# Optimization experiments

Hardware: AMD Instinct MI355X
Metric: run time of the kernel (lower is better)

The kernel has to match this reference:

```python
import jax, jax.numpy as jnp
import numpy as np

FEAT_STRIDE = 16
PRE_NMS_TOP_N = 4000
POST_NMS_TOP_N = 300
NMS_THRESH = 0.7


def _whctrs(a):
    w = a[2] - a[0] + 1.0
    h = a[3] - a[1] + 1.0
    return w, h, a[0] + 0.5 * (w - 1.0), a[1] + 0.5 * (h - 1.0)

def _mkanchors(ws, hs, xc, yc):
    ws = ws[:, None]; hs = hs[:, None]
    return np.hstack([xc - 0.5 * (ws - 1), yc - 0.5 * (hs - 1), xc + 0.5 * (ws - 1), yc + 0.5 * (hs - 1)])

def _ratio_enum(anchor, ratios):
    w, h, xc, yc = _whctrs(anchor)
    size = w * h
    ws = np.round(np.sqrt(size / ratios))
    hs = np.round(ws * ratios)
    return _mkanchors(ws, hs, xc, yc)

def _scale_enum(anchor, scales):
    w, h, xc, yc = _whctrs(anchor)
    return _mkanchors(w * scales, h * scales, xc, yc)

def generate_anchors(base_size, ratios, scales):
    base = np.array([1.0, 1.0, base_size, base_size], dtype=np.float64) - 1.0
    ra = _ratio_enum(base, np.asarray(ratios, dtype=np.float64))
    return np.vstack([_scale_enum(ra[i], np.asarray(scales, dtype=np.float64)) for i in range(ra.shape[0])]).astype(np.float32)

# ---- NMS: sequential greedy suppression over score-sorted boxes ----

def _nms_keep(boxes, thresh):
    # boxes: [N,4] sorted by descending score. Legacy +1 area convention.
    boxes = jax.lax.stop_gradient(boxes)
    x1, y1, x2, y2 = boxes[:, 0], boxes[:, 1], boxes[:, 2], boxes[:, 3]
    areas = (x2 - x1 + 1.0) * (y2 - y1 + 1.0)
    xx1 = jnp.maximum(x1[:, None], x1[None, :])
    yy1 = jnp.maximum(y1[:, None], y1[None, :])
    xx2 = jnp.minimum(x2[:, None], x2[None, :])
    yy2 = jnp.minimum(y2[:, None], y2[None, :])
    w = jnp.maximum(xx2 - xx1 + 1.0, 0.0)
    h = jnp.maximum(yy2 - yy1 + 1.0, 0.0)
    inter = w * h
    iou = inter / (areas[:, None] + areas[None, :] - inter)
    sup = iou > thresh  # [N,N]
    n = boxes.shape[0]
    idxs = jnp.arange(n)

    def body(suppressed, i):
        kept = ~suppressed[i]
        suppressed = suppressed | (kept & sup[i] & (idxs > i))
        return suppressed, kept

    _, keep = jax.lax.scan(body, jnp.zeros((n,), dtype=bool), idxs)
    return keep  # [N] bool

# ---- forward ----

def _forward(scores, bbox_deltas, im_info, anchors):
    A = anchors.shape[0]
    B = bbox_deltas.shape[0]
    H, W = scores.shape[2], scores.shape[3]
    sc = scores[:, A:, :, :]  # fg scores [B,A,H,W]

    # anchor grid: K = H*W shifts, anchors broadcast over shifts (K major, A minor)
    shift_x = jnp.arange(W, dtype=scores.dtype) * FEAT_STRIDE
    shift_y = jnp.arange(H, dtype=scores.dtype) * FEAT_STRIDE
    sx, sy = jnp.meshgrid(shift_x, shift_y)  # 'xy' indexing, like np.meshgrid
    shifts = jnp.stack([sx.ravel(), sy.ravel(), sx.ravel(), sy.ravel()], axis=1)  # [K,4]
    all_anchors = (anchors[None, :, :] + shifts[:, None, :]).reshape(-1, 4)  # [K*A,4]

    deltas = bbox_deltas.transpose(0, 2, 3, 1).reshape(B, -1, 4)  # [B,N,4]
    scr = sc.transpose(0, 2, 3, 1).reshape(B, -1)  # [B,N]

    # bbox_transform_inv
    widths = all_anchors[:, 2] - all_anchors[:, 0] + 1.0
    heights = all_anchors[:, 3] - all_anchors[:, 1] + 1.0
    ctr_x = all_anchors[:, 0] + 0.5 * widths
    ctr_y = all_anchors[:, 1] + 0.5 * heights
    dx, dy, dw, dh = deltas[..., 0], deltas[..., 1], deltas[..., 2], deltas[..., 3]
    pcx = dx * widths + ctr_x
    pcy = dy * heights + ctr_y
    pw = jnp.exp(dw) * widths
    ph = jnp.exp(dh) * heights
    px1 = pcx - 0.5 * pw
    py1 = pcy - 0.5 * ph
    px2 = pcx + 0.5 * pw
    py2 = pcy + 0.5 * ph

    # clip_boxes per image: x in [0, W_img-1], y in [0, H_img-1]
    wmax = im_info[:, 1:2] - 1.0  # [B,1]
    hmax = im_info[:, 0:1] - 1.0
    px1 = jnp.clip(px1, 0.0, wmax)
    px2 = jnp.clip(px2, 0.0, wmax)
    py1 = jnp.clip(py1, 0.0, hmax)
    py2 = jnp.clip(py2, 0.0, hmax)
    proposals = jnp.stack([px1, py1, px2, py2], axis=-1)  # [B,N,4]

    def per_image(props, s, b_idx):
        _, order = jax.lax.top_k(s, PRE_NMS_TOP_N)  # descending
        p = props[order]  # [PRE,4]
        keep = _nms_keep(p, NMS_THRESH)
        ranks = jnp.cumsum(keep.astype(jnp.int32)) - 1
        slot = jnp.where(keep & (ranks < POST_NMS_TOP_N), ranks, POST_NMS_TOP_N)
        boxes_out = jnp.zeros((POST_NMS_TOP_N + 1, 4), p.dtype).at[slot].set(p)[:POST_NMS_TOP_N]
        col0 = jnp.full((POST_NMS_TOP_N, 1), b_idx.astype(p.dtype))
        return jnp.concatenate([col0, boxes_out], axis=1)  # [POST,5]

    return jax.vmap(per_image)(proposals, scr, jnp.arange(B))


def setup_inputs() -> dict:
    key = jax.random.key(0)
    k1, k2 = jax.random.split(key)
    B, A, H, W = 2, 9, 50, 50
    scores = jax.random.normal(k1, (B, 2 * A, H, W), dtype=jnp.float32)
    bbox_deltas = jax.random.normal(k2, (B, 4 * A, H, W), dtype=jnp.float32) * 0.1
    im_info = jnp.tile(jnp.array([[800.0, 800.0, 1.0]], dtype=jnp.float32), (B, 1))
    anchors = jnp.asarray(generate_anchors(16, [0.5, 1.0, 2.0], [8, 16, 32]))
    return {"scores": scores, "bbox_deltas": bbox_deltas, "im_info": im_info, "anchors": anchors}


def reference(scores, bbox_deltas, im_info, anchors):
    return _forward(scores, bbox_deltas, im_info, anchors)
```

## Files before the change

kernel.cpp:

```cpp
#include <hip/hip_runtime.h>
#include <stdint.h>

#define NA 9
#define HH 50
#define WW 50
#define NPROP (HH*WW*NA)
#define PRE_NMS 4000
#define POST_NMS 300
#define NWORDS 63
#define ROWSTRIDE 64
#define MROWS 4032
#define SORTN 8192
#define NMS_T 0.7f
#define FSTRIDE 16.0f

typedef unsigned long long ull;

__device__ __forceinline__ uint32_t f32_ord(float s) {
    uint32_t u = __float_as_uint(s);
    return (u & 0x80000000u) ? ~u : (u | 0x80000000u);
}

__global__ void decode_hist(const float* __restrict__ scores,
                            const float* __restrict__ deltas,
                            const float* __restrict__ im_info,
                            const float* __restrict__ anchors,
                            ull* __restrict__ keys,
                            float4* __restrict__ boxes4,
                            uint32_t* __restrict__ hist, int B) {
    int t = blockIdx.x * blockDim.x + threadIdx.x;
    if (t >= B * NPROP) return;
    int b = t / NPROP;
    int i = t % NPROP;

    int a   = i % NA;
    int pos = i / NA;
    int w   = pos % WW;
    int h   = pos / WW;

    float score = scores[((size_t)b*2*NA + NA + a)*(HH*WW) + pos];
    ull key = ((ull)f32_ord(score) << 32) | (ull)(0xFFFFFFFFu - (uint32_t)i);
    keys[t] = key;
    atomicAdd(&hist[((uint32_t)b << 16) | (uint32_t)(key >> 48)], 1u);

    float ax1 = anchors[a*4+0], ay1 = anchors[a*4+1];
    float ax2 = anchors[a*4+2], ay2 = anchors[a*4+3];
    float sx = (float)w * FSTRIDE, sy = (float)h * FSTRIDE;
    float x1 = ax1 + sx, y1 = ay1 + sy, x2 = ax2 + sx, y2 = ay2 + sy;
    float bw = x2 - x1 + 1.0f;
    float bh = y2 - y1 + 1.0f;
    float cx = x1 + 0.5f * bw;
    float cy = y1 + 0.5f * bh;

    const float* dp = deltas + (size_t)b*4*NA*(HH*WW);
    float dx = dp[(4*a+0)*(HH*WW)+pos];
    float dy = dp[(4*a+1)*(HH*WW)+pos];
    float dw = dp[(4*a+2)*(HH*WW)+pos];
    float dh = dp[(4*a+3)*(HH*WW)+pos];

    float pcx = dx * bw + cx;
    float pcy = dy * bh + cy;
    float pw  = expf(dw) * bw;
    float ph  = expf(dh) * bh;

    float wmax = im_info[b*3+1] - 1.0f;
    float hmax = im_info[b*3+0] - 1.0f;
    float px1 = fminf(fmaxf(pcx - 0.5f*pw, 0.0f), wmax);
    float py1 = fminf(fmaxf(pcy - 0.5f*ph, 0.0f), hmax);
    float px2 = fminf(fmaxf(pcx + 0.5f*pw, 0.0f), wmax);
    float py2 = fminf(fmaxf(pcy + 0.5f*ph, 0.0f), hmax);

    boxes4[t] = make_float4(px1, py1, px2, py2);
}

__global__ __launch_bounds__(1024) void select_sort_gather(
        const ull* __restrict__ keys,
        const uint32_t* __restrict__ hist,
        const float4* __restrict__ boxes4,
        float4* __restrict__ gboxes) {
    __shared__ ull sk[SORTN];
    __shared__ int sA[1024], sB[1024];
    __shared__ int nfine[64];
    __shared__ int sSeg, aboveC, thr, lcount;
    int img = blockIdx.x, tid = threadIdx.x;
    const uint32_t* h = hist + ((uint32_t)img << 16);

    {
        const uint4* h4 = (const uint4*)h;
        uint32_t s = 0;
        #pragma unroll
        for (int u = 0; u < 16; ++u) {
            uint4 v = h4[(tid << 4) | u];
            s += v.x + v.y + v.z + v.w;
        }
        sA[tid] = (int)s;
    }
    __syncthreads();
    int* curp = sA; int* nxtp = sB;
    for (int d = 1; d < 1024; d <<= 1) {
        int v = curp[tid] + ((tid + d < 1024) ? curp[tid + d] : 0);
        nxtp[tid] = v;
        __syncthreads();
        int* tmp = curp; curp = nxtp; nxtp = tmp;
    }
    {
        int cftS  = curp[tid];
        int cftS1 = (tid < 1023) ? curp[tid + 1] : 0;
        if (cftS >= PRE_NMS && cftS1 < PRE_NMS) { sSeg = tid; aboveC = cftS1; }
    }
    __syncthreads();
    if (tid < 64) nfine[tid] = (int)h[(sSeg << 6) | tid];
    __syncthreads();
    if (tid == 0) {
        int cum = aboveC;
        int t = sSeg << 6;
        for (int w = 63; w >= 0; --w) {
            int nc = cum + nfine[w];
            if (nc >= PRE_NMS) { t = (sSeg << 6) | w; break; }
            cum = nc;
        }
        thr = t;
        lcount = 0;
    }
    __syncthreads();

    {
        const ull* kb = keys + (size_t)img * NPROP;
        int th = thr;
        for (int i = tid; i < NPROP; i += 1024) {
            ull key = kb[i];
            if ((int)(key >> 48) >= th) {
                int p = atomicAdd(&lcount, 1);
                if (p < SORTN) sk[p] = key;
            }
        }
    }
    __syncthreads();
    {
        int M = lcount;
        for (int e = tid; e < SORTN; e += 1024)
            if (e >= M) sk[e] = 0ull;
    }
    __syncthreads();

    for (int k = 2; k <= SORTN; k <<= 1) {
        for (int j = k >> 1; j > 0; j >>= 1) {
            for (int p = tid; p < SORTN/2; p += 1024) {
                int i2 = ((p & ~(j-1)) << 1) | (p & (j-1));
                int l2 = i2 | j;
                bool desc = ((i2 & k) == 0);
                ull x = sk[i2], y = sk[l2];
                if ((x < y) == desc) { sk[i2] = y; sk[l2] = x; }
            }
            __syncthreads();
        }
    }

    for (int e = tid; e < PRE_NMS; e += 1024) {
        uint32_t idx = 0xFFFFFFFFu - (uint32_t)(sk[e] & 0xFFFFFFFFull);
        gboxes[(size_t)img*PRE_NMS + e] = boxes4[(size_t)img*NPROP + idx];
    }
}

__global__ __launch_bounds__(64) void mask_kernel(const float4* __restrict__ gboxes,
                                                  ull* __restrict__ mask) {
    int rb = blockIdx.x, cb = blockIdx.y, b = blockIdx.z;
    if (cb < rb) return;
    __shared__ float cx1[64], cy1[64], cx2[64], cy2[64], car[64];
    int tid = threadIdx.x;

    int j0 = cb*64 + tid;
    float4 cbx = (j0 < PRE_NMS) ? gboxes[(size_t)b*PRE_NMS + j0]
                                : make_float4(0.f,0.f,0.f,0.f);
    cx1[tid]=cbx.x; cy1[tid]=cbx.y; cx2[tid]=cbx.z; cy2[tid]=cbx.w;
    car[tid]=(cbx.z-cbx.x+1.0f)*(cbx.w-cbx.y+1.0f);
    __syncthreads();

    int i = rb*64 + tid;
    if (i >= PRE_NMS) return;
    float4 rbx = gboxes[(size_t)b*PRE_NMS + i];
    float ix1=rbx.x, iy1=rbx.y, ix2=rbx.z, iy2=rbx.w;
    float iarea=(ix2-ix1+1.0f)*(iy2-iy1+1.0f);

    ull bits = 0;
    #pragma unroll 16
    for (int k = 0; k < 64; ++k) {
        int j = cb*64 + k;
        float xx1 = fmaxf(ix1, cx1[k]);
        float yy1 = fmaxf(iy1, cy1[k]);
        float xx2 = fminf(ix2, cx2[k]);
        float yy2 = fminf(iy2, cy2[k]);
        float ww = fmaxf(xx2 - xx1 + 1.0f, 0.0f);
        float hh = fmaxf(yy2 - yy1 + 1.0f, 0.0f);
        float inter = ww * hh;
        float iou = inter / (iarea + car[k] - inter);
        if ((j > i) & (j < PRE_NMS) & (iou > NMS_T)) bits |= (1ull << k);
    }
    mask[(((size_t)b*MROWS + i) << 6) + cb] = bits;
}

__global__ __launch_bounds__(64) void scan_kernel(const ull* __restrict__ mask,
                                                  const float4* __restrict__ gboxes,
                                                  float* __restrict__ out) {
    __shared__ ull buf[2][64][ROWSTRIDE];
    __shared__ int keep_idx[POST_NMS];
    int b = blockIdx.x;
    int lane = threadIdx.x;
    const ull* mbase = mask + ((size_t)b * MROWS << 6);

    ull supp = 0;
    if (lane == NWORDS-1) supp = 0xFFFFFFFF00000000ull;
    if (lane >= NWORDS)   supp = ~0ull;
    int kept = 0;
    bool done = false;
    int cur = 0;

    {
        const ulonglong2* src = (const ulonglong2*)mbase;
        ulonglong2* d2 = (ulonglong2*)buf[0];
        #pragma unroll
        for (int m = 0; m < 32; ++m) d2[lane + (m << 6)] = src[lane + (m << 6)];
        __syncthreads();
    }

    for (int wi = 0; wi < NWORDS && !done; ++wi) {
        ulonglong2 pf[32];
        bool havepf = (wi + 1 < NWORDS);
        if (havepf) {
            const ulonglong2* src =
                (const ulonglong2*)(mbase + (((size_t)(wi+1) << 6) << 6));
            #pragma unroll
            for (int m = 0; m < 32; ++m) pf[m] = src[lane + (m << 6)];
        }

        ull avail = ~__shfl(supp, wi);
        while (avail) {
            int bi = __builtin_ctzll(avail);
            int i = (wi << 6) + bi;
            if (lane == 0) keep_idx[kept] = i;
            ++kept;
            if (kept >= POST_NMS) { done = true; break; }
            ull w = buf[cur][bi][wi];
            ull r = (lane > wi) ? buf[cur][bi][lane] : 0;
            supp |= r;
            avail &= ~w;
            avail &= ~(1ull << bi);
        }

        if (havepf && !done) {
            ulonglong2* d2 = (ulonglong2*)buf[cur ^ 1];
            #pragma unroll
            for (int m = 0; m < 32; ++m) d2[lane + (m << 6)] = pf[m];
            __syncthreads();
            cur ^= 1;
        }
    }
    __syncthreads();

    for (int r = lane; r < POST_NMS; r += 64) {
        float4 bx = (r < kept) ? gboxes[(size_t)b*PRE_NMS + keep_idx[r]]
                               : make_float4(0.f,0.f,0.f,0.f);
        float* o = out + (size_t)(b*POST_NMS + r)*5;
        o[0]=(float)b; o[1]=bx.x; o[2]=bx.y; o[3]=bx.z; o[4]=bx.w;
    }
}

extern "C" void kernel_launch(void* const* d_in, const int* in_sizes, int n_in,
                              void* d_out, int out_size, void* d_ws, size_t ws_size,
                              hipStream_t stream) {
    (void)n_in; (void)out_size; (void)ws_size;
    const float* scores  = (const float*)d_in[0];
    const float* deltas  = (const float*)d_in[1];
    const float* im_info = (const float*)d_in[2];
    const float* anchors = (const float*)d_in[3];
    float* out = (float*)d_out;

    const int B = in_sizes[0] / (2*NA*HH*WW);

    float4* boxes4 = (float4*)d_ws;
    float4* gboxes = boxes4 + (size_t)B*NPROP;
    ull*    keys   = (ull*)(gboxes + (size_t)B*PRE_NMS);
    ull*    mask   = keys + (size_t)B*NPROP;
    uint32_t* hist = (uint32_t*)(mask + ((size_t)B*MROWS << 6));

    hipMemsetAsync(hist, 0, (size_t)B*65536*sizeof(uint32_t), stream);
    decode_hist<<<(B*NPROP + 255)/256, 256, 0, stream>>>(scores, deltas, im_info,
                                                         anchors, keys, boxes4, hist, B);
    select_sort_gather<<<B, 1024, 0, stream>>>(keys, hist, boxes4, gboxes);
    dim3 mgrid(NWORDS, NWORDS, B);
    mask_kernel<<<mgrid, 64, 0, stream>>>(gboxes, mask);
    scan_kernel<<<B, 64, 0, stream>>>(mask, gboxes, out);
}
```

Before: 256.8 us.

## Replace single-block bitonic sort with multi-block rank-by-counting scatter

The single 1024-thread block per image that compacted candidate keys and bitonic-sorted 8192 entries in shared memory is split into two kernels. A compact kernel writes candidate keys to global memory, and a rank_scatter kernel spreads across up to 32 blocks per image. Each thread computes its key's rank by comparing against all candidates, then scatters its box to that rank. This replaces many barrier-bound sort stages on two blocks with O(M^2) parallel comparisons across more CUs. The cost is an extra launch and a global round trip for the keys.

```diff
diff --git a/kernel.cpp b/kernel.cpp
--- a/kernel.cpp
+++ b/kernel.cpp
@@ -10,7 +10,7 @@
 #define NWORDS 63
 #define ROWSTRIDE 64
 #define MROWS 4032
-#define SORTN 8192
+#define SELN 8192
 #define NMS_T 0.7f
 #define FSTRIDE 16.0f
 
@@ -73,12 +73,11 @@
     boxes4[t] = make_float4(px1, py1, px2, py2);
 }
 
-__global__ __launch_bounds__(1024) void select_sort_gather(
+__global__ __launch_bounds__(1024) void compact_kernel(
         const ull* __restrict__ keys,
         const uint32_t* __restrict__ hist,
-        const float4* __restrict__ boxes4,
-        float4* __restrict__ gboxes) {
-    __shared__ ull sk[SORTN];
+        ull* __restrict__ ckeys,
+        int* __restrict__ mcount) {
     __shared__ int sA[1024], sB[1024];
     __shared__ int nfine[64];
     __shared__ int sSeg, aboveC, thr, lcount;
@@ -124,6 +123,7 @@
     }
     __syncthreads();
 
+    ull* ck = ckeys + (size_t)img * SELN;
     {
         const ull* kb = keys + (size_t)img * NPROP;
         int th = thr;
@@ -131,34 +131,45 @@
             ull key = kb[i];
             if ((int)(key >> 48) >= th) {
                 int p = atomicAdd(&lcount, 1);
-                if (p < SORTN) sk[p] = key;
+                if (p < SELN) ck[p] = key;
             }
         }
     }
     __syncthreads();
-    {
-        int M = lcount;
-        for (int e = tid; e < SORTN; e += 1024)
-            if (e >= M) sk[e] = 0ull;
-    }
-    __syncthreads();
-
-    for (int k = 2; k <= SORTN; k <<= 1) {
-        for (int j = k >> 1; j > 0; j >>= 1) {
-            for (int p = tid; p < SORTN/2; p += 1024) {
-                int i2 = ((p & ~(j-1)) << 1) | (p & (j-1));
-                int l2 = i2 | j;
-                bool desc = ((i2 & k) == 0);
-                ull x = sk[i2], y = sk[l2];
-                if ((x < y) == desc) { sk[i2] = y; sk[l2] = x; }
-            }
-            __syncthreads();
-        }
-    }
-
-    for (int e = tid; e < PRE_NMS; e += 1024) {
-        uint32_t idx = 0xFFFFFFFFu - (uint32_t)(sk[e] & 0xFFFFFFFFull);
-        gboxes[(size_t)img*PRE_NMS + e] = boxes4[(size_t)img*NPROP + idx];
+    int M = lcount; if (M > SELN) M = SELN;
+    if (tid == 0) mcount[img] = M;
+    for (int e = M + tid; e < SELN; e += 1024) ck[e] = 0ull;
+}
+
+__global__ __launch_bounds__(256) void rank_scatter(
+        const ull* __restrict__ ckeys,
+        const int* __restrict__ mcount,
+        const float4* __restrict__ boxes4,
+        float4* __restrict__ gboxes) {
+    __shared__ ull lk[SELN];
+    __shared__ int sM;
+    int img = blockIdx.y, rb = blockIdx.x, tid = threadIdx.x;
+    if (tid == 0) sM = mcount[img];
+    __syncthreads();
+    int M = sM;
+    if (rb * 256 >= M) return;
+    int Ms = (M + 255) & ~255;
+
+    const ull* kb = ckeys + (size_t)img * SELN;
+    for (int e = tid; e < Ms; e += 256) lk[e] = (e < M) ? kb[e] : 0ull;
+    __syncthreads();
+
+    int row = rb * 256 + tid;
+    if (row >= M) return;
+    ull my = lk[row];
+
+    int rank = 0;
+    #pragma unroll 8
+    for (int e = 0; e < Ms; ++e) rank += (lk[e] > my) ? 1 : 0;
+
+    if (rank < PRE_NMS) {
+        uint32_t idx = 0xFFFFFFFFu - (uint32_t)(my & 0xFFFFFFFFull);
+        gboxes[(size_t)img*PRE_NMS + rank] = boxes4[(size_t)img*NPROP + idx];
     }
 }
 
@@ -280,13 +291,17 @@
     float4* boxes4 = (float4*)d_ws;
     float4* gboxes = boxes4 + (size_t)B*NPROP;
     ull*    keys   = (ull*)(gboxes + (size_t)B*PRE_NMS);
-    ull*    mask   = keys + (size_t)B*NPROP;
+    ull*    ckeys  = keys + (size_t)B*NPROP;
+    ull*    mask   = ckeys + (size_t)B*SELN;
     uint32_t* hist = (uint32_t*)(mask + ((size_t)B*MROWS << 6));
+    int*    mcount = (int*)(hist + (size_t)B*65536);
 
     hipMemsetAsync(hist, 0, (size_t)B*65536*sizeof(uint32_t), stream);
     decode_hist<<<(B*NPROP + 255)/256, 256, 0, stream>>>(scores, deltas, im_info,
                                                          anchors, keys, boxes4, hist, B);
-    select_sort_gather<<<B, 1024, 0, stream>>>(keys, hist, boxes4, gboxes);
+    compact_kernel<<<B, 1024, 0, stream>>>(keys, hist, ckeys, mcount);
+    dim3 rgrid(SELN/256, B);
+    rank_scatter<<<rgrid, 256, 0, stream>>>(ckeys, mcount, boxes4, gboxes);
     dim3 mgrid(NWORDS, NWORDS, B);
     mask_kernel<<<mgrid, 64, 0, stream>>>(gboxes, mask);
     scan_kernel<<<B, 64, 0, stream>>>(mask, gboxes, out);
```

Result: faster. 249.8 us (-2.7%).
